# Kernel tuning notes

Measured on AMD Instinct MI355X. Metric: run time of the kernel, lower is better.

## Reference

```python
import jax, jax.numpy as jnp
import numpy as np

B, N, F = 32, 512, 128
AGG, FCH, NCLS, NLAYER = 128, 256, 10, 3


def setup_inputs() -> dict:
    key = jax.random.key(0)
    ks = jax.random.split(key, 10)
    s = 1.0 / np.sqrt(F)
    inp = {
        "x": jax.random.normal(ks[0], (B, N, F), jnp.float32),
        "L_re": jax.random.normal(ks[1], (B, N, N), jnp.float32) / np.sqrt(N),
        "L_im": jax.random.normal(ks[2], (B, N, N), jnp.float32) / np.sqrt(N),
        # stacked complex layer weights (layer0: F->AGG, rest AGG->AGG; F==AGG)
        "Wr": jax.random.normal(ks[3], (NLAYER, F, AGG), jnp.float32) * s,
        "Wi": jax.random.normal(ks[4], (NLAYER, F, AGG), jnp.float32) * s,
        "fc1_w": jax.random.normal(ks[5], (FCH, 2 * AGG), jnp.float32) / np.sqrt(2 * AGG),
        "fc1_b": jnp.zeros((FCH,), jnp.float32),
        "fc2_w": jax.random.normal(ks[6], (NCLS, FCH), jnp.float32) / np.sqrt(FCH),
        "fc2_b": jnp.zeros((NCLS,), jnp.float32),
    }
    return inp


def reference(x, L_re, L_im, Wr, Wi, fc1_w, fc1_b, fc2_w, fc2_b):
    L = jax.lax.complex(L_re, L_im)                      # [B,N,N] complex magnetic Laplacian
    h = x.astype(jnp.complex64)                          # x + 0j, [B,N,F]
    for i in range(NLAYER):
        W = jax.lax.complex(Wr[i], Wi[i])                # [F,AGG] complex
        h = jnp.einsum('bnm,bmf->bnf', L, h)             # complex aggregation
        h = jnp.einsum('bnf,fo->bno', h, W)              # complex transform
        # complex ReLU: keep z where Re(z) >= 0, else 0 (vectorized mask-multiply)
        h = jnp.where(jnp.real(h) >= 0, h, jnp.zeros((), h.dtype))
        # dropout skipped (eval mode)
    # readout: mean over nodes, concat real & imag -> [B, 2*AGG]
    p = jnp.mean(h, axis=1)
    feat = jnp.concatenate([jnp.real(p), jnp.imag(p)], axis=-1)
    z = jax.nn.relu(feat @ fc1_w.T + fc1_b)
    logits = z @ fc2_w.T + fc2_b
    return jax.nn.softmax(logits, axis=-1)
```

## Files before the change

kernel.cpp:

```cpp
#include <hip/hip_runtime.h>
#include <hip/hip_bf16.h>
#include <math.h>

#define B_SZ   32
#define N_SZ   512
#define F_SZ   128

typedef __attribute__((ext_vector_type(8))) short short8v;
typedef __attribute__((ext_vector_type(4))) short short4v;
typedef __attribute__((ext_vector_type(4))) float f32x4;

typedef const __attribute__((address_space(1))) unsigned int* gas1_t;
typedef __attribute__((address_space(3))) unsigned int* las3_t;
#define GLD16(gsrc, ldst) __builtin_amdgcn_global_load_lds( \
    (gas1_t)(const void*)(gsrc), (las3_t)(unsigned int)(size_t)(void*)(ldst), 16, 0, 0)

__device__ __forceinline__ short bfh(float v) {
    __hip_bfloat16 h = __float2bfloat16(v);
    return __builtin_bit_cast(short, h);
}
__device__ __forceinline__ float bf2f(short s) {
    unsigned u = ((unsigned)(unsigned short)s) << 16;
    return __builtin_bit_cast(float, u);
}
__device__ __forceinline__ void split1(float v, short& h, short& l) {
    short hs = bfh(v);
    h = hs;
    l = bfh(v - bf2f(hs));
}

__device__ __forceinline__ void splitpack(const float4& a, const float4& b,
                                          short8v& h, short8v& l) {
    const float va[8] = {a.x, a.y, a.z, a.w, b.x, b.y, b.z, b.w};
    #pragma unroll
    for (int j = 0; j < 8; ++j) {
        short hs, ls;
        split1(va[j], hs, ls);
        h[j] = hs; l[j] = ls;
    }
}

template<int HAS_BIM, int EPI>
__global__ __launch_bounds__(512, 2)
void cgemm_mfma(const float* __restrict__ Ar, const float* __restrict__ Ai,
                long sA, int lda,
                const short* __restrict__ Brh, const short* __restrict__ Brl,
                const short* __restrict__ Bih, const short* __restrict__ Bil,
                long sB, int ldb, int K,
                float* __restrict__ Cr, float* __restrict__ Ci, long sC,
                short* __restrict__ Orh, short* __restrict__ Orl,
                short* __restrict__ Oih, short* __restrict__ Oil)
{
    __shared__ short As[4][64 * 64];
    __shared__ short Bs[4][128 * 64];

    const int t = threadIdx.x;
    const int b = blockIdx.y;
    const int rowBase = blockIdx.x * 64;

    const float* ArB = Ar + (long)b * sA;
    const float* AiB = Ai + (long)b * sA;
    const short* BrhB = Brh + (long)b * sB;
    const short* BrlB = Brl + (long)b * sB;
    const short* BihB = HAS_BIM ? (Bih + (long)b * sB) : nullptr;
    const short* BilB = HAS_BIM ? (Bil + (long)b * sB) : nullptr;

    const int ra = t >> 3;
    const int ca = t & 7;
    const int aslot = ca ^ (ra & 7);

    const int w = t >> 6, l = t & 63;
    const int wm = w >> 2, wn = w & 3;
    const int r16 = l & 15, g = l >> 4;

    const f32x4 z4 = {0.f, 0.f, 0.f, 0.f};
    f32x4 accR[2][2], accI[2][2];
    #pragma unroll
    for (int i = 0; i < 2; ++i)
        #pragma unroll
        for (int j = 0; j < 2; ++j) { accR[i][j] = z4; accI[i][j] = z4; }

    short8v SGN;
    #pragma unroll
    for (int j = 0; j < 8; ++j) SGN[j] = (short)0x8000;

    for (int kb = 0; kb < K; kb += 64) {
        #pragma unroll
        for (int rep = 0; rep < 2; ++rep) {
            const int i = t + rep * 512;
            const int n = i >> 3, cb = i & 7;
            const long srcoff = (long)n * ldb + kb + 8 * (cb ^ (n & 7));
            GLD16(BrhB + srcoff, &Bs[0][i * 8]);
            GLD16(BrlB + srcoff, &Bs[1][i * 8]);
            if (HAS_BIM) {
                GLD16(BihB + srcoff, &Bs[2][i * 8]);
                GLD16(BilB + srcoff, &Bs[3][i * 8]);
            }
        }
        {
            const float* ar_ = ArB + (long)(rowBase + ra) * lda + kb + ca * 8;
            const float* ai_ = AiB + (long)(rowBase + ra) * lda + kb + ca * 8;
            float4 x0 = *(const float4*)ar_;
            float4 x1 = *(const float4*)(ar_ + 4);
            float4 y0 = *(const float4*)ai_;
            float4 y1 = *(const float4*)(ai_ + 4);
            short8v h8, l8;
            splitpack(x0, x1, h8, l8);
            *(short8v*)&As[0][ra * 64 + 8 * aslot] = h8;
            *(short8v*)&As[1][ra * 64 + 8 * aslot] = l8;
            splitpack(y0, y1, h8, l8);
            *(short8v*)&As[2][ra * 64 + 8 * aslot] = h8;
            *(short8v*)&As[3][ra * 64 + 8 * aslot] = l8;
        }
        __syncthreads();

        #pragma unroll
        for (int w4 = 0; w4 < 2; ++w4) {
            short8v fArh[2], fArl[2], fAih[2], fAil[2];
            short8v fBrh[2], fBrl[2], fBih[2], fBil[2];
            #pragma unroll
            for (int tm = 0; tm < 2; ++tm) {
                const int r = wm * 32 + tm * 16 + r16;
                const int off = r * 64 + 8 * ((w4 * 4 + g) ^ (r & 7));
                fArh[tm] = *(const short8v*)&As[0][off];
                fArl[tm] = *(const short8v*)&As[1][off];
                fAih[tm] = *(const short8v*)&As[2][off];
                fAil[tm] = *(const short8v*)&As[3][off];
            }
            #pragma unroll
            for (int tn = 0; tn < 2; ++tn) {
                const int n = wn * 32 + tn * 16 + r16;
                const int off = n * 64 + 8 * ((w4 * 4 + g) ^ (n & 7));
                fBrh[tn] = *(const short8v*)&Bs[0][off];
                fBrl[tn] = *(const short8v*)&Bs[1][off];
                if (HAS_BIM) {
                    fBih[tn] = *(const short8v*)&Bs[2][off];
                    fBil[tn] = *(const short8v*)&Bs[3][off];
                }
            }
            #pragma unroll
            for (int tm = 0; tm < 2; ++tm) {
                const short8v nIh = fAih[tm] ^ SGN;
                const short8v nIl = fAil[tm] ^ SGN;
                #pragma unroll
                for (int tn = 0; tn < 2; ++tn) {
                    accR[tm][tn] = __builtin_amdgcn_mfma_f32_16x16x32_bf16(fArh[tm], fBrh[tn], accR[tm][tn], 0, 0, 0);
                    accR[tm][tn] = __builtin_amdgcn_mfma_f32_16x16x32_bf16(fArl[tm], fBrh[tn], accR[tm][tn], 0, 0, 0);
                    accR[tm][tn] = __builtin_amdgcn_mfma_f32_16x16x32_bf16(fArh[tm], fBrl[tn], accR[tm][tn], 0, 0, 0);
                    if (HAS_BIM) {
                        accR[tm][tn] = __builtin_amdgcn_mfma_f32_16x16x32_bf16(nIh, fBih[tn], accR[tm][tn], 0, 0, 0);
                        accR[tm][tn] = __builtin_amdgcn_mfma_f32_16x16x32_bf16(nIl, fBih[tn], accR[tm][tn], 0, 0, 0);
                        accR[tm][tn] = __builtin_amdgcn_mfma_f32_16x16x32_bf16(nIh, fBil[tn], accR[tm][tn], 0, 0, 0);
                    }
                    accI[tm][tn] = __builtin_amdgcn_mfma_f32_16x16x32_bf16(fAih[tm], fBrh[tn], accI[tm][tn], 0, 0, 0);
                    accI[tm][tn] = __builtin_amdgcn_mfma_f32_16x16x32_bf16(fAil[tm], fBrh[tn], accI[tm][tn], 0, 0, 0);
                    accI[tm][tn] = __builtin_amdgcn_mfma_f32_16x16x32_bf16(fAih[tm], fBrl[tn], accI[tm][tn], 0, 0, 0);
                    if (HAS_BIM) {
                        accI[tm][tn] = __builtin_amdgcn_mfma_f32_16x16x32_bf16(fArh[tm], fBih[tn], accI[tm][tn], 0, 0, 0);
                        accI[tm][tn] = __builtin_amdgcn_mfma_f32_16x16x32_bf16(fArl[tm], fBih[tn], accI[tm][tn], 0, 0, 0);
                        accI[tm][tn] = __builtin_amdgcn_mfma_f32_16x16x32_bf16(fArh[tm], fBil[tn], accI[tm][tn], 0, 0, 0);
                    }
                }
            }
        }
        __syncthreads();
    }

    #pragma unroll
    for (int tm = 0; tm < 2; ++tm) {
        #pragma unroll
        for (int tn = 0; tn < 2; ++tn) {
            f32x4 vr = accR[tm][tn], vi = accI[tm][tn];
            const int m0 = rowBase + wm * 32 + tm * 16 + 4 * g;
            const int n0 = wn * 32 + tn * 16 + r16;
            if (EPI == 0) {
                #pragma unroll
                for (int rr = 0; rr < 4; ++rr) {
                    Cr[(long)b * sC + (long)(m0 + rr) * 128 + n0] = vr[rr];
                    Ci[(long)b * sC + (long)(m0 + rr) * 128 + n0] = vi[rr];
                }
            } else {
                short4v rh, rl, ih, il;
                #pragma unroll
                for (int rr = 0; rr < 4; ++rr) {
                    float cr = vr[rr], cim = vi[rr];
                    if (cr < 0.f) { cr = 0.f; cim = 0.f; }
                    short hs, ls;
                    split1(cr, hs, ls);  rh[rr] = hs; rl[rr] = ls;
                    split1(cim, hs, ls); ih[rr] = hs; il[rr] = ls;
                }
                const long base = ((long)b * 128 + n0) * 512 + m0;
                *(short4v*)(Orh + base) = rh;
                *(short4v*)(Orl + base) = rl;
                *(short4v*)(Oih + base) = ih;
                *(short4v*)(Oil + base) = il;
            }
        }
    }
}

__global__ __launch_bounds__(256)
void split_x_kernel(const float* __restrict__ x, short* __restrict__ Xh,
                    short* __restrict__ Xl)
{
    __shared__ float XT[128][65];
    const int b = blockIdx.x >> 3, nc = blockIdx.x & 7;
    const int t = threadIdx.x;
    {
        const int nl = t & 63, fc = t >> 6;
        const float* src = x + ((long)b * 512 + nc * 64 + nl) * 128 + fc * 32;
        #pragma unroll
        for (int q = 0; q < 8; ++q) {
            float4 v = *(const float4*)(src + q * 4);
            XT[fc * 32 + q * 4 + 0][nl] = v.x;
            XT[fc * 32 + q * 4 + 1][nl] = v.y;
            XT[fc * 32 + q * 4 + 2][nl] = v.z;
            XT[fc * 32 + q * 4 + 3][nl] = v.w;
        }
    }
    __syncthreads();
    const int f = t >> 1, half = t & 1;
    short8v H[4], L[4];
    #pragma unroll
    for (int i = 0; i < 32; ++i) {
        short hs, ls;
        split1(XT[f][half * 32 + i], hs, ls);
        H[i >> 3][i & 7] = hs;
        L[i >> 3][i & 7] = ls;
    }
    const long base = ((long)b * 128 + f) * 512 + nc * 64 + half * 32;
    #pragma unroll
    for (int q = 0; q < 4; ++q) {
        *(short8v*)(Xh + base + q * 8) = H[q];
        *(short8v*)(Xl + base + q * 8) = L[q];
    }
}

__global__ __launch_bounds__(128)
void split_w_kernel(const float* __restrict__ Wr, const float* __restrict__ Wi,
                    short* __restrict__ Wrh, short* __restrict__ Wrl,
                    short* __restrict__ Wih, short* __restrict__ Wil)
{
    const int layer = blockIdx.x >> 7, n = blockIdx.x & 127;
    const int k = threadIdx.x;
    const long src = ((long)layer * 128 + k) * 128 + n;
    const long dst = ((long)layer * 128 + n) * 128 + k;
    short hs, ls;
    split1(Wr[src], hs, ls); Wrh[dst] = hs; Wrl[dst] = ls;
    split1(Wi[src], hs, ls); Wih[dst] = hs; Wil[dst] = ls;
}

__global__ __launch_bounds__(256)
void readout_kernel(const short* __restrict__ Hrh, const short* __restrict__ Hrl,
                    const short* __restrict__ Hih, const short* __restrict__ Hil,
                    float* __restrict__ part)
{
    const int b = blockIdx.x >> 3, nc = blockIdx.x & 7;
    const int t = threadIdx.x;
    const int f = t & 127;
    const short* Ph = (t < 128) ? Hrh : Hih;
    const short* Pl = (t < 128) ? Hrl : Hil;
    const long base = ((long)b * 128 + f) * 512 + nc * 64;
    float s = 0.f;
    #pragma unroll
    for (int q = 0; q < 8; ++q) {
        short8v vh = *(const short8v*)(Ph + base + q * 8);
        short8v vl = *(const short8v*)(Pl + base + q * 8);
        #pragma unroll
        for (int j = 0; j < 8; ++j) s += bf2f(vh[j]) + bf2f(vl[j]);
    }
    part[((long)b * 8 + nc) * 256 + t] = s;
}

__global__ __launch_bounds__(256)
void head_kernel(const float* __restrict__ part,
                 const float* __restrict__ w1, const float* __restrict__ b1,
                 const float* __restrict__ w2, const float* __restrict__ b2,
                 float* __restrict__ out)
{
    __shared__ float sf[256];
    __shared__ float sz[256];
    __shared__ float sl[16];
    const int b = blockIdx.x;
    const int t = threadIdx.x;

    float s = 0.f;
    #pragma unroll
    for (int nc = 0; nc < 8; ++nc) s += part[((long)b * 8 + nc) * 256 + t];
    sf[t] = s * (1.0f / 512.0f);
    __syncthreads();

    float acc = b1[t];
    const float* wrow = w1 + (long)t * 256;
    #pragma unroll 8
    for (int j = 0; j < 256; ++j) acc = fmaf(sf[j], wrow[j], acc);
    sz[t] = fmaxf(acc, 0.f);
    __syncthreads();

    if (t < 10) {
        float lg = b2[t];
        const float* w2r = w2 + (long)t * 256;
        #pragma unroll 8
        for (int j = 0; j < 256; ++j) lg = fmaf(sz[j], w2r[j], lg);
        sl[t] = lg;
    }
    __syncthreads();
    if (t == 0) {
        float m = sl[0];
        for (int c = 1; c < 10; ++c) m = fmaxf(m, sl[c]);
        float e[10]; float ss = 0.f;
        for (int c = 0; c < 10; ++c) { e[c] = expf(sl[c] - m); ss += e[c]; }
        const float inv = 1.f / ss;
        for (int c = 0; c < 10; ++c) out[b * 10 + c] = e[c] * inv;
    }
}

extern "C" void kernel_launch(void* const* d_in, const int* in_sizes, int n_in,
                              void* d_out, int out_size, void* d_ws, size_t ws_size,
                              hipStream_t stream)
{
    const float* x     = (const float*)d_in[0];
    const float* Lre   = (const float*)d_in[1];
    const float* Lim   = (const float*)d_in[2];
    const float* Wr    = (const float*)d_in[3];
    const float* Wi    = (const float*)d_in[4];
    const float* fc1_w = (const float*)d_in[5];
    const float* fc1_b = (const float*)d_in[6];
    const float* fc2_w = (const float*)d_in[7];
    const float* fc2_b = (const float*)d_in[8];
    float* out = (float*)d_out;

    const long BNF = (long)B_SZ * N_SZ * F_SZ;
    float* Tre = (float*)d_ws;
    float* Tim = Tre + BNF;
    short* Hrh = (short*)(Tim + BNF);
    short* Hrl = Hrh + BNF;
    short* Hih = Hrl + BNF;
    short* Hil = Hih + BNF;
    short* Wrh = Hil + BNF;
    short* Wrl = Wrh + 3 * 128 * 128;
    short* Wih = Wrl + 3 * 128 * 128;
    short* Wil = Wih + 3 * 128 * 128;
    float* part = (float*)(Wil + 3 * 128 * 128);

    const long sL = (long)N_SZ * N_SZ;
    const long sH = (long)F_SZ * N_SZ;
    const dim3 ggrid(8, 32);

    split_w_kernel<<<384, 128, 0, stream>>>(Wr, Wi, Wrh, Wrl, Wih, Wil);
    split_x_kernel<<<256, 256, 0, stream>>>(x, Hrh, Hrl);

    for (int layer = 0; layer < 3; ++layer) {
        if (layer == 0) {
            cgemm_mfma<0, 0><<<ggrid, 512, 0, stream>>>(
                Lre, Lim, sL, 512, Hrh, Hrl, nullptr, nullptr, sH, 512, 512,
                Tre, Tim, sH, nullptr, nullptr, nullptr, nullptr);
        } else {
            cgemm_mfma<1, 0><<<ggrid, 512, 0, stream>>>(
                Lre, Lim, sL, 512, Hrh, Hrl, Hih, Hil, sH, 512, 512,
                Tre, Tim, sH, nullptr, nullptr, nullptr, nullptr);
        }
        const long wo = (long)layer * 128 * 128;
        cgemm_mfma<1, 1><<<ggrid, 512, 0, stream>>>(
            Tre, Tim, sH, 128, Wrh + wo, Wrl + wo, Wih + wo, Wil + wo, 0, 128, 128,
            nullptr, nullptr, 0, Hrh, Hrl, Hih, Hil);
    }

    readout_kernel<<<256, 256, 0, stream>>>(Hrh, Hrl, Hih, Hil, part);
    head_kernel<<<32, 256, 0, stream>>>(part, fc1_w, fc1_b, fc2_w, fc2_b, out);
}
```

Baseline: 290.8 us.

## Fuse aggregation and weight transform into one kernel per layer with double-buffered pipeline

Each layer now runs as one kernel. The L·H aggregation tile (32 nodes × 128 features) is kept in LDS as split bf16 hi/lo and immediately multiplied by the complex weight, so the fp32 T intermediate no longer makes a round trip through global memory and there are fewer launches. The K loop is double-buffered: B tiles go through global_load_lds and A (L) values are loaded straight into registers for the next step while MFMAs run on the current one. Blocks are 256 threads covering 32 rows, with a remapped block index, and activations ping-pong between two workspace buffers. The cost is that the small W GEMM is recomputed per 32-row tile, with W fragments read from global memory, and each block covers fewer rows.

```diff
diff --git a/kernel.cpp b/kernel.cpp
--- a/kernel.cpp
+++ b/kernel.cpp
@@ -15,6 +15,8 @@
 #define GLD16(gsrc, ldst) __builtin_amdgcn_global_load_lds( \
     (gas1_t)(const void*)(gsrc), (las3_t)(unsigned int)(size_t)(void*)(ldst), 16, 0, 0)
 
+#define MFMA16(a, bb, c) __builtin_amdgcn_mfma_f32_16x16x32_bf16((a), (bb), (c), 0, 0, 0)
+
 __device__ __forceinline__ short bfh(float v) {
     __hip_bfloat16 h = __float2bfloat16(v);
     return __builtin_bit_cast(short, h);
@@ -28,7 +30,6 @@
     h = hs;
     l = bfh(v - bf2f(hs));
 }
-
 __device__ __forceinline__ void splitpack(const float4& a, const float4& b,
                                           short8v& h, short8v& l) {
     const float va[8] = {a.x, a.y, a.z, a.w, b.x, b.y, b.z, b.w};
@@ -40,38 +41,41 @@
     }
 }
 
-template<int HAS_BIM, int EPI>
-__global__ __launch_bounds__(512, 2)
-void cgemm_mfma(const float* __restrict__ Ar, const float* __restrict__ Ai,
-                long sA, int lda,
-                const short* __restrict__ Brh, const short* __restrict__ Brl,
-                const short* __restrict__ Bih, const short* __restrict__ Bil,
-                long sB, int ldb, int K,
-                float* __restrict__ Cr, float* __restrict__ Ci, long sC,
-                short* __restrict__ Orh, short* __restrict__ Orl,
-                short* __restrict__ Oih, short* __restrict__ Oil)
-{
-    __shared__ short As[4][64 * 64];
-    __shared__ short Bs[4][128 * 64];
+template<int HAS_BIM>
+__global__ __launch_bounds__(256, 2)
+void fused_layer(const float* __restrict__ Lre, const float* __restrict__ Lim,
+                 const short* __restrict__ Brh, const short* __restrict__ Brl,
+                 const short* __restrict__ Bih, const short* __restrict__ Bil,
+                 const short* __restrict__ Wrh, const short* __restrict__ Wrl,
+                 const short* __restrict__ Wih, const short* __restrict__ Wil,
+                 short* __restrict__ Orh, short* __restrict__ Orl,
+                 short* __restrict__ Oih, short* __restrict__ Oil)
+{
+    __shared__ __align__(16) char ldsraw[65536];
+    short (*Bs)[4][4096] = (short(*)[4][4096])ldsraw;
+    short (*Ts)[32 * 136] = (short(*)[32 * 136])ldsraw;
 
     const int t = threadIdx.x;
-    const int b = blockIdx.y;
-    const int rowBase = blockIdx.x * 64;
-
-    const float* ArB = Ar + (long)b * sA;
-    const float* AiB = Ai + (long)b * sA;
-    const short* BrhB = Brh + (long)b * sB;
-    const short* BrlB = Brl + (long)b * sB;
-    const short* BihB = HAS_BIM ? (Bih + (long)b * sB) : nullptr;
-    const short* BilB = HAS_BIM ? (Bil + (long)b * sB) : nullptr;
-
-    const int ra = t >> 3;
-    const int ca = t & 7;
-    const int aslot = ca ^ (ra & 7);
-
-    const int w = t >> 6, l = t & 63;
-    const int wm = w >> 2, wn = w & 3;
+    const int lid = blockIdx.y * 16 + blockIdx.x;
+    const int nl = (lid & 7) * 64 + (lid >> 3);
+    const int b = nl >> 4;
+    const int rowBase = (nl & 15) * 32;
+
+    const float* pLre = Lre + (long)b * (N_SZ * N_SZ);
+    const float* pLim = Lim + (long)b * (N_SZ * N_SZ);
+    const long sB = (long)F_SZ * N_SZ;
+    const short* pBrh = Brh + (long)b * sB;
+    const short* pBrl = Brl + (long)b * sB;
+    const short* pBih = HAS_BIM ? (Bih + (long)b * sB) : nullptr;
+    const short* pBil = HAS_BIM ? (Bil + (long)b * sB) : nullptr;
+
+    const int wn = t >> 6;
+    const int l = t & 63;
     const int r16 = l & 15, g = l >> 4;
+
+    short8v SGN;
+    #pragma unroll
+    for (int j = 0; j < 8; ++j) SGN[j] = (short)0x8000;
 
     const f32x4 z4 = {0.f, 0.f, 0.f, 0.f};
     f32x4 accR[2][2], accI[2][2];
@@ -80,123 +84,186 @@
         #pragma unroll
         for (int j = 0; j < 2; ++j) { accR[i][j] = z4; accI[i][j] = z4; }
 
-    short8v SGN;
-    #pragma unroll
-    for (int j = 0; j < 8; ++j) SGN[j] = (short)0x8000;
-
-    for (int kb = 0; kb < K; kb += 64) {
-        #pragma unroll
-        for (int rep = 0; rep < 2; ++rep) {
-            const int i = t + rep * 512;
-            const int n = i >> 3, cb = i & 7;
-            const long srcoff = (long)n * ldb + kb + 8 * (cb ^ (n & 7));
-            GLD16(BrhB + srcoff, &Bs[0][i * 8]);
-            GLD16(BrlB + srcoff, &Bs[1][i * 8]);
-            if (HAS_BIM) {
-                GLD16(BihB + srcoff, &Bs[2][i * 8]);
-                GLD16(BilB + srcoff, &Bs[3][i * 8]);
+#define STAGE_B(buf, kb)                                                     \
+    {                                                                        \
+        _Pragma("unroll")                                                    \
+        for (int rep = 0; rep < 2; ++rep) {                                  \
+            const int i_ = t + rep * 256;                                    \
+            const int n_ = i_ >> 2, s_ = i_ & 3;                             \
+            const int c_ = s_ ^ ((n_ >> 1) & 3);                             \
+            const long so_ = (long)n_ * 512 + (kb) + 8 * c_;                 \
+            GLD16(pBrh + so_, &Bs[buf][0][i_ * 8]);                          \
+            GLD16(pBrl + so_, &Bs[buf][1][i_ * 8]);                          \
+            if (HAS_BIM) {                                                   \
+                GLD16(pBih + so_, &Bs[buf][2][i_ * 8]);                      \
+                GLD16(pBil + so_, &Bs[buf][3][i_ * 8]);                      \
+            }                                                                \
+        }                                                                    \
+    }
+
+#define LOAD_A(R, kb)                                                        \
+    {                                                                        \
+        _Pragma("unroll")                                                    \
+        for (int tm_ = 0; tm_ < 2; ++tm_) {                                  \
+            const long ro_ = (long)(rowBase + tm_ * 16 + r16) * 512 + (kb) + g * 8; \
+            R[tm_][0][0] = *(const float4*)(pLre + ro_);                     \
+            R[tm_][0][1] = *(const float4*)(pLre + ro_ + 4);                 \
+            R[tm_][1][0] = *(const float4*)(pLim + ro_);                     \
+            R[tm_][1][1] = *(const float4*)(pLim + ro_ + 4);                 \
+        }                                                                    \
+    }
+
+#define STEP(buf, R)                                                         \
+    {                                                                        \
+        short8v FA[2][4];                                                    \
+        _Pragma("unroll")                                                    \
+        for (int tm_ = 0; tm_ < 2; ++tm_) {                                  \
+            splitpack(R[tm_][0][0], R[tm_][0][1], FA[tm_][0], FA[tm_][1]);   \
+            splitpack(R[tm_][1][0], R[tm_][1][1], FA[tm_][2], FA[tm_][3]);   \
+        }                                                                    \
+        short8v fB[2][4];                                                    \
+        _Pragma("unroll")                                                    \
+        for (int tn_ = 0; tn_ < 2; ++tn_) {                                  \
+            const int n_ = wn * 32 + tn_ * 16 + r16;                         \
+            const int off_ = n_ * 32 + 8 * (g ^ ((n_ >> 1) & 3));            \
+            fB[tn_][0] = *(const short8v*)&Bs[buf][0][off_];                 \
+            fB[tn_][1] = *(const short8v*)&Bs[buf][1][off_];                 \
+            if (HAS_BIM) {                                                   \
+                fB[tn_][2] = *(const short8v*)&Bs[buf][2][off_];             \
+                fB[tn_][3] = *(const short8v*)&Bs[buf][3][off_];             \
+            }                                                                \
+        }                                                                    \
+        _Pragma("unroll")                                                    \
+        for (int tm_ = 0; tm_ < 2; ++tm_) {                                  \
+            const short8v nIh_ = FA[tm_][2] ^ SGN;                           \
+            const short8v nIl_ = FA[tm_][3] ^ SGN;                           \
+            _Pragma("unroll")                                                \
+            for (int tn_ = 0; tn_ < 2; ++tn_) {                              \
+                accR[tm_][tn_] = MFMA16(FA[tm_][0], fB[tn_][0], accR[tm_][tn_]); \
+                accR[tm_][tn_] = MFMA16(FA[tm_][1], fB[tn_][0], accR[tm_][tn_]); \
+                accR[tm_][tn_] = MFMA16(FA[tm_][0], fB[tn_][1], accR[tm_][tn_]); \
+                accI[tm_][tn_] = MFMA16(FA[tm_][2], fB[tn_][0], accI[tm_][tn_]); \
+                accI[tm_][tn_] = MFMA16(FA[tm_][3], fB[tn_][0], accI[tm_][tn_]); \
+                accI[tm_][tn_] = MFMA16(FA[tm_][2], fB[tn_][1], accI[tm_][tn_]); \
+                if (HAS_BIM) {                                               \
+                    accR[tm_][tn_] = MFMA16(nIh_, fB[tn_][2], accR[tm_][tn_]);   \
+                    accR[tm_][tn_] = MFMA16(nIl_, fB[tn_][2], accR[tm_][tn_]);   \
+                    accR[tm_][tn_] = MFMA16(nIh_, fB[tn_][3], accR[tm_][tn_]);   \
+                    accI[tm_][tn_] = MFMA16(FA[tm_][0], fB[tn_][2], accI[tm_][tn_]); \
+                    accI[tm_][tn_] = MFMA16(FA[tm_][1], fB[tn_][2], accI[tm_][tn_]); \
+                    accI[tm_][tn_] = MFMA16(FA[tm_][0], fB[tn_][3], accI[tm_][tn_]); \
+                }                                                            \
+            }                                                                \
+        }                                                                    \
+    }
+
+    float4 Ra[2][2][2], Rb[2][2][2];
+    STAGE_B(0, 0);
+    LOAD_A(Ra, 0);
+    __syncthreads();
+
+    for (int k2 = 0; k2 < 8; ++k2) {
+        const int kb = k2 * 64;
+        STAGE_B(1, kb + 32);
+        LOAD_A(Rb, kb + 32);
+        STEP(0, Ra);
+        __syncthreads();
+        if (k2 < 7) {
+            STAGE_B(0, kb + 64);
+            LOAD_A(Ra, kb + 64);
+        }
+        STEP(1, Rb);
+        __syncthreads();
+    }
+
+    #pragma unroll
+    for (int tm = 0; tm < 2; ++tm)
+        #pragma unroll
+        for (int tn = 0; tn < 2; ++tn) {
+            const int f = wn * 32 + tn * 16 + r16;
+            #pragma unroll
+            for (int rr = 0; rr < 4; ++rr) {
+                const int node = tm * 16 + 4 * g + rr;
+                short hs, ls;
+                split1(accR[tm][tn][rr], hs, ls);
+                Ts[0][node * 136 + f] = hs; Ts[1][node * 136 + f] = ls;
+                split1(accI[tm][tn][rr], hs, ls);
+                Ts[2][node * 136 + f] = hs; Ts[3][node * 136 + f] = ls;
             }
         }
-        {
-            const float* ar_ = ArB + (long)(rowBase + ra) * lda + kb + ca * 8;
-            const float* ai_ = AiB + (long)(rowBase + ra) * lda + kb + ca * 8;
-            float4 x0 = *(const float4*)ar_;
-            float4 x1 = *(const float4*)(ar_ + 4);
-            float4 y0 = *(const float4*)ai_;
-            float4 y1 = *(const float4*)(ai_ + 4);
-            short8v h8, l8;
-            splitpack(x0, x1, h8, l8);
-            *(short8v*)&As[0][ra * 64 + 8 * aslot] = h8;
-            *(short8v*)&As[1][ra * 64 + 8 * aslot] = l8;
-            splitpack(y0, y1, h8, l8);
-            *(short8v*)&As[2][ra * 64 + 8 * aslot] = h8;
-            *(short8v*)&As[3][ra * 64 + 8 * aslot] = l8;
-        }
-        __syncthreads();
-
-        #pragma unroll
-        for (int w4 = 0; w4 < 2; ++w4) {
-            short8v fArh[2], fArl[2], fAih[2], fAil[2];
-            short8v fBrh[2], fBrl[2], fBih[2], fBil[2];
+    __syncthreads();
+
+    f32x4 acc2R[2][2], acc2I[2][2];
+    #pragma unroll
+    for (int i = 0; i < 2; ++i)
+        #pragma unroll
+        for (int j = 0; j < 2; ++j) { acc2R[i][j] = z4; acc2I[i][j] = z4; }
+
+    #pragma unroll
+    for (int c = 0; c < 4; ++c) {
+        short8v fW[2][4];
+        #pragma unroll
+        for (int tn = 0; tn < 2; ++tn) {
+            const long wo = (long)(wn * 32 + tn * 16 + r16) * 128 + c * 32 + g * 8;
+            fW[tn][0] = *(const short8v*)(Wrh + wo);
+            fW[tn][1] = *(const short8v*)(Wrl + wo);
+            fW[tn][2] = *(const short8v*)(Wih + wo);
+            fW[tn][3] = *(const short8v*)(Wil + wo);
+        }
+        short8v fT[2][4];
+        #pragma unroll
+        for (int tm = 0; tm < 2; ++tm) {
+            const int off = (tm * 16 + r16) * 136 + c * 32 + g * 8;
             #pragma unroll
-            for (int tm = 0; tm < 2; ++tm) {
-                const int r = wm * 32 + tm * 16 + r16;
-                const int off = r * 64 + 8 * ((w4 * 4 + g) ^ (r & 7));
-                fArh[tm] = *(const short8v*)&As[0][off];
-                fArl[tm] = *(const short8v*)&As[1][off];
-                fAih[tm] = *(const short8v*)&As[2][off];
-                fAil[tm] = *(const short8v*)&As[3][off];
-            }
+            for (int p = 0; p < 4; ++p)
+                fT[tm][p] = *(const short8v*)&Ts[p][off];
+        }
+        #pragma unroll
+        for (int tm = 0; tm < 2; ++tm) {
+            const short8v nIh = fT[tm][2] ^ SGN;
+            const short8v nIl = fT[tm][3] ^ SGN;
             #pragma unroll
             for (int tn = 0; tn < 2; ++tn) {
-                const int n = wn * 32 + tn * 16 + r16;
-                const int off = n * 64 + 8 * ((w4 * 4 + g) ^ (n & 7));
-                fBrh[tn] = *(const short8v*)&Bs[0][off];
-                fBrl[tn] = *(const short8v*)&Bs[1][off];
-                if (HAS_BIM) {
-                    fBih[tn] = *(const short8v*)&Bs[2][off];
-                    fBil[tn] = *(const short8v*)&Bs[3][off];
-                }
+                acc2R[tm][tn] = MFMA16(fT[tm][0], fW[tn][0], acc2R[tm][tn]);
+                acc2R[tm][tn] = MFMA16(fT[tm][1], fW[tn][0], acc2R[tm][tn]);
+                acc2R[tm][tn] = MFMA16(fT[tm][0], fW[tn][1], acc2R[tm][tn]);
+                acc2R[tm][tn] = MFMA16(nIh, fW[tn][2], acc2R[tm][tn]);
+                acc2R[tm][tn] = MFMA16(nIl, fW[tn][2], acc2R[tm][tn]);
+                acc2R[tm][tn] = MFMA16(nIh, fW[tn][3], acc2R[tm][tn]);
+                acc2I[tm][tn] = MFMA16(fT[tm][2], fW[tn][0], acc2I[tm][tn]);
+                acc2I[tm][tn] = MFMA16(fT[tm][3], fW[tn][0], acc2I[tm][tn]);
+                acc2I[tm][tn] = MFMA16(fT[tm][2], fW[tn][1], acc2I[tm][tn]);
+                acc2I[tm][tn] = MFMA16(fT[tm][0], fW[tn][2], acc2I[tm][tn]);
+                acc2I[tm][tn] = MFMA16(fT[tm][1], fW[tn][2], acc2I[tm][tn]);
+                acc2I[tm][tn] = MFMA16(fT[tm][0], fW[tn][3], acc2I[tm][tn]);
             }
+        }
+    }
+
+    #pragma unroll
+    for (int tm = 0; tm < 2; ++tm)
+        #pragma unroll
+        for (int tn = 0; tn < 2; ++tn) {
+            const int out = wn * 32 + tn * 16 + r16;
+            const int node0 = rowBase + tm * 16 + 4 * g;
+            short4v rh, rl, ih, il;
             #pragma unroll
-            for (int tm = 0; tm < 2; ++tm) {
-                const short8v nIh = fAih[tm] ^ SGN;
-                const short8v nIl = fAil[tm] ^ SGN;
-                #pragma unroll
-                for (int tn = 0; tn < 2; ++tn) {
-                    accR[tm][tn] = __builtin_amdgcn_mfma_f32_16x16x32_bf16(fArh[tm], fBrh[tn], accR[tm][tn], 0, 0, 0);
-                    accR[tm][tn] = __builtin_amdgcn_mfma_f32_16x16x32_bf16(fArl[tm], fBrh[tn], accR[tm][tn], 0, 0, 0);
-                    accR[tm][tn] = __builtin_amdgcn_mfma_f32_16x16x32_bf16(fArh[tm], fBrl[tn], accR[tm][tn], 0, 0, 0);
-                    if (HAS_BIM) {
-                        accR[tm][tn] = __builtin_amdgcn_mfma_f32_16x16x32_bf16(nIh, fBih[tn], accR[tm][tn], 0, 0, 0);
-                        accR[tm][tn] = __builtin_amdgcn_mfma_f32_16x16x32_bf16(nIl, fBih[tn], accR[tm][tn], 0, 0, 0);
-                        accR[tm][tn] = __builtin_amdgcn_mfma_f32_16x16x32_bf16(nIh, fBil[tn], accR[tm][tn], 0, 0, 0);
-                    }
-                    accI[tm][tn] = __builtin_amdgcn_mfma_f32_16x16x32_bf16(fAih[tm], fBrh[tn], accI[tm][tn], 0, 0, 0);
-                    accI[tm][tn] = __builtin_amdgcn_mfma_f32_16x16x32_bf16(fAil[tm], fBrh[tn], accI[tm][tn], 0, 0, 0);
-                    accI[tm][tn] = __builtin_amdgcn_mfma_f32_16x16x32_bf16(fAih[tm], fBrl[tn], accI[tm][tn], 0, 0, 0);
-                    if (HAS_BIM) {
-                        accI[tm][tn] = __builtin_amdgcn_mfma_f32_16x16x32_bf16(fArh[tm], fBih[tn], accI[tm][tn], 0, 0, 0);
-                        accI[tm][tn] = __builtin_amdgcn_mfma_f32_16x16x32_bf16(fArl[tm], fBih[tn], accI[tm][tn], 0, 0, 0);
-                        accI[tm][tn] = __builtin_amdgcn_mfma_f32_16x16x32_bf16(fArh[tm], fBil[tn], accI[tm][tn], 0, 0, 0);
-                    }
-                }
+            for (int rr = 0; rr < 4; ++rr) {
+                float cr = acc2R[tm][tn][rr], ci = acc2I[tm][tn][rr];
+                if (cr < 0.f) { cr = 0.f; ci = 0.f; }
+                short hs, ls;
+                split1(cr, hs, ls); rh[rr] = hs; rl[rr] = ls;
+                split1(ci, hs, ls); ih[rr] = hs; il[rr] = ls;
             }
-        }
-        __syncthreads();
-    }
-
-    #pragma unroll
-    for (int tm = 0; tm < 2; ++tm) {
-        #pragma unroll
-        for (int tn = 0; tn < 2; ++tn) {
-            f32x4 vr = accR[tm][tn], vi = accI[tm][tn];
-            const int m0 = rowBase + wm * 32 + tm * 16 + 4 * g;
-            const int n0 = wn * 32 + tn * 16 + r16;
-            if (EPI == 0) {
-                #pragma unroll
-                for (int rr = 0; rr < 4; ++rr) {
-                    Cr[(long)b * sC + (long)(m0 + rr) * 128 + n0] = vr[rr];
-                    Ci[(long)b * sC + (long)(m0 + rr) * 128 + n0] = vi[rr];
-                }
-            } else {
-                short4v rh, rl, ih, il;
-                #pragma unroll
-                for (int rr = 0; rr < 4; ++rr) {
-                    float cr = vr[rr], cim = vi[rr];
-                    if (cr < 0.f) { cr = 0.f; cim = 0.f; }
-                    short hs, ls;
-                    split1(cr, hs, ls);  rh[rr] = hs; rl[rr] = ls;
-                    split1(cim, hs, ls); ih[rr] = hs; il[rr] = ls;
-                }
-                const long base = ((long)b * 128 + n0) * 512 + m0;
-                *(short4v*)(Orh + base) = rh;
-                *(short4v*)(Orl + base) = rl;
-                *(short4v*)(Oih + base) = ih;
-                *(short4v*)(Oil + base) = il;
-            }
-        }
-    }
+            const long base = ((long)b * 128 + out) * 512 + node0;
+            *(short4v*)(Orh + base) = rh;
+            *(short4v*)(Orl + base) = rl;
+            *(short4v*)(Oih + base) = ih;
+            *(short4v*)(Oil + base) = il;
+        }
+#undef STAGE_B
+#undef LOAD_A
+#undef STEP
 }
 
 __global__ __launch_bounds__(256)
@@ -207,15 +274,15 @@
     const int b = blockIdx.x >> 3, nc = blockIdx.x & 7;
     const int t = threadIdx.x;
     {
-        const int nl = t & 63, fc = t >> 6;
-        const float* src = x + ((long)b * 512 + nc * 64 + nl) * 128 + fc * 32;
+        const int nlan = t & 63, fc = t >> 6;
+        const float* src = x + ((long)b * 512 + nc * 64 + nlan) * 128 + fc * 32;
         #pragma unroll
         for (int q = 0; q < 8; ++q) {
             float4 v = *(const float4*)(src + q * 4);
-            XT[fc * 32 + q * 4 + 0][nl] = v.x;
-            XT[fc * 32 + q * 4 + 1][nl] = v.y;
-            XT[fc * 32 + q * 4 + 2][nl] = v.z;
-            XT[fc * 32 + q * 4 + 3][nl] = v.w;
+            XT[fc * 32 + q * 4 + 0][nlan] = v.x;
+            XT[fc * 32 + q * 4 + 1][nlan] = v.y;
+            XT[fc * 32 + q * 4 + 2][nlan] = v.z;
+            XT[fc * 32 + q * 4 + 3][nlan] = v.w;
         }
     }
     __syncthreads();
@@ -331,41 +398,34 @@
     float* out = (float*)d_out;
 
     const long BNF = (long)B_SZ * N_SZ * F_SZ;
-    float* Tre = (float*)d_ws;
-    float* Tim = Tre + BNF;
-    short* Hrh = (short*)(Tim + BNF);
-    short* Hrl = Hrh + BNF;
-    short* Hih = Hrl + BNF;
-    short* Hil = Hih + BNF;
-    short* Wrh = Hil + BNF;
+    short* h0 = (short*)d_ws;
+    short* h1 = h0 + 4 * BNF;
+    short* Wrh = h1 + 4 * BNF;
     short* Wrl = Wrh + 3 * 128 * 128;
     short* Wih = Wrl + 3 * 128 * 128;
     short* Wil = Wih + 3 * 128 * 128;
     float* part = (float*)(Wil + 3 * 128 * 128);
 
-    const long sL = (long)N_SZ * N_SZ;
-    const long sH = (long)F_SZ * N_SZ;
-    const dim3 ggrid(8, 32);
+    const dim3 ggrid(16, 32);
+    const long wsz = 128 * 128;
 
     split_w_kernel<<<384, 128, 0, stream>>>(Wr, Wi, Wrh, Wrl, Wih, Wil);
-    split_x_kernel<<<256, 256, 0, stream>>>(x, Hrh, Hrl);
-
-    for (int layer = 0; layer < 3; ++layer) {
-        if (layer == 0) {
-            cgemm_mfma<0, 0><<<ggrid, 512, 0, stream>>>(
-                Lre, Lim, sL, 512, Hrh, Hrl, nullptr, nullptr, sH, 512, 512,
-                Tre, Tim, sH, nullptr, nullptr, nullptr, nullptr);
-        } else {
-            cgemm_mfma<1, 0><<<ggrid, 512, 0, stream>>>(
-                Lre, Lim, sL, 512, Hrh, Hrl, Hih, Hil, sH, 512, 512,
-                Tre, Tim, sH, nullptr, nullptr, nullptr, nullptr);
-        }
-        const long wo = (long)layer * 128 * 128;
-        cgemm_mfma<1, 1><<<ggrid, 512, 0, stream>>>(
-            Tre, Tim, sH, 128, Wrh + wo, Wrl + wo, Wih + wo, Wil + wo, 0, 128, 128,
-            nullptr, nullptr, 0, Hrh, Hrl, Hih, Hil);
-    }
-
-    readout_kernel<<<256, 256, 0, stream>>>(Hrh, Hrl, Hih, Hil, part);
+    split_x_kernel<<<256, 256, 0, stream>>>(x, h0, h0 + BNF);
+
+    fused_layer<0><<<ggrid, 256, 0, stream>>>(
+        Lre, Lim, h0, h0 + BNF, nullptr, nullptr,
+        Wrh, Wrl, Wih, Wil,
+        h1, h1 + BNF, h1 + 2 * BNF, h1 + 3 * BNF);
+    fused_layer<1><<<ggrid, 256, 0, stream>>>(
+        Lre, Lim, h1, h1 + BNF, h1 + 2 * BNF, h1 + 3 * BNF,
+        Wrh + wsz, Wrl + wsz, Wih + wsz, Wil + wsz,
+        h0, h0 + BNF, h0 + 2 * BNF, h0 + 3 * BNF);
+    fused_layer<1><<<ggrid, 256, 0, stream>>>(
+        Lre, Lim, h0, h0 + BNF, h0 + 2 * BNF, h0 + 3 * BNF,
+        Wrh + 2 * wsz, Wrl + 2 * wsz, Wih + 2 * wsz, Wil + 2 * wsz,
+        h1, h1 + BNF, h1 + 2 * BNF, h1 + 3 * BNF);
+
+    readout_kernel<<<256, 256, 0, stream>>>(
+        h1, h1 + BNF, h1 + 2 * BNF, h1 + 3 * BNF, part);
     head_kernel<<<32, 256, 0, stream>>>(part, fc1_w, fc1_b, fc2_w, fc2_b, out);
 }
```

Result: slower. 302.4 us (+4.0%).
